# Kernel optimization log

Hardware: AMD Instinct MI355X
Metric: run time of the kernel (lower is better)

The kernel has to match this reference:

```python
import jax, jax.numpy as jnp
from jax import lax
import numpy as np

K_TOP = 100
NMS_THRESH = 0.5
SUBJECT_CATEGORY_ID = 0


def box_cxcywh_to_xyxy(b):
    cx, cy, w, h = b[..., 0], b[..., 1], b[..., 2], b[..., 3]
    return jnp.stack([cx - 0.5 * w, cy - 0.5 * h, cx + 0.5 * w, cy + 0.5 * h], axis=-1)


def _pairwise_iou(boxes):
    # boxes: [K,4] xyxy; uses the +1 pixel convention from the original numpy NMS
    x1, y1, x2, y2 = boxes[:, 0], boxes[:, 1], boxes[:, 2], boxes[:, 3]
    area = (x2 - x1 + 1.0) * (y2 - y1 + 1.0)
    xx1 = jnp.maximum(x1[:, None], x1[None, :])
    yy1 = jnp.maximum(y1[:, None], y1[None, :])
    xx2 = jnp.minimum(x2[:, None], x2[None, :])
    yy2 = jnp.minimum(y2[:, None], y2[None, :])
    w = jnp.maximum(0.0, xx2 - xx1 + 1.0)
    h = jnp.maximum(0.0, yy2 - yy1 + 1.0)
    inter = w * h
    union = area[:, None] + area[None, :] - inter
    return inter / union


def _nms_keep(sub_boxes, obj_boxes, obj_labels, hoi_scores):
    # Greedy grouped pairwise NMS for one image.
    # Grouping key degenerates to object label (subject cat and verb-row are constant).
    K = sub_boxes.shape[0]
    max_scores = hoi_scores.max(axis=-1)
    order = jnp.argsort(-max_scores)
    ovr = _pairwise_iou(sub_boxes) * _pairwise_iou(obj_boxes)  # [K,K]
    same_group = obj_labels[:, None] == obj_labels[None, :]
    ovr = jnp.where(same_group, ovr, 0.0)
    ovr_s = ovr[order][:, order]
    upper = jnp.triu(jnp.ones((K, K), dtype=bool), k=1)
    sup_mat = (ovr_s > NMS_THRESH) & upper  # suppression only of later (lower-score) items

    def body(i, st):
        suppressed, keep = st
        ki = jnp.logical_not(suppressed[i])
        keep = keep.at[i].set(ki)
        suppressed = suppressed | (ki & sup_mat[i])
        return suppressed, keep

    _, keep_sorted = lax.fori_loop(0, K, body, (jnp.zeros(K, bool), jnp.zeros(K, bool)))
    return jnp.zeros(K, bool).at[order].set(keep_sorted)


def setup_inputs() -> dict:
    key = jax.random.key(0)
    k1, k2, k3, k4, k5, k6 = jax.random.split(key, 6)
    B, Q, C, V = 256, 300, 81, 117
    return {
        "pred_obj_logits": jax.random.normal(k1, (B, Q, C), dtype=jnp.float32),
        "pred_verb_logits": jax.random.normal(k2, (B, Q, V), dtype=jnp.float32),
        "pred_sub_boxes": jax.random.uniform(k3, (B, Q, 4), dtype=jnp.float32),
        "pred_obj_boxes": jax.random.uniform(k4, (B, Q, 4), dtype=jnp.float32),
        "correct_mat": (jax.random.uniform(k5, (V, C), dtype=jnp.float32) > 0.3).astype(jnp.float32),
        "target_sizes": jax.random.randint(k6, (B, 2), 200, 640, dtype=jnp.int32),
    }


def reference(pred_obj_logits, pred_verb_logits, pred_sub_boxes, pred_obj_boxes, correct_mat, target_sizes):
    B, Q, C = pred_obj_logits.shape
    V = pred_verb_logits.shape[-1]

    obj_prob = jax.nn.softmax(pred_obj_logits, axis=-1)       # [B,Q,C]  (no_obj=False)
    verb_scores = jax.nn.sigmoid(pred_verb_logits)            # [B,Q,V]

    topk_values, topk_indexes = lax.top_k(obj_prob.reshape(B, Q * C), K_TOP)  # [B,100]
    topk_boxes = topk_indexes // C
    obj_labels = topk_indexes % C

    vs = jnp.take_along_axis(verb_scores, topk_boxes[..., None], axis=1)      # [B,100,V]
    ob = jnp.take_along_axis(pred_obj_boxes, topk_boxes[..., None], axis=1)   # [B,100,4]
    sb = jnp.take_along_axis(pred_sub_boxes, topk_boxes[..., None], axis=1)

    img_h = target_sizes[:, 0].astype(jnp.float32)
    img_w = target_sizes[:, 1].astype(jnp.float32)
    scale_fct = jnp.stack([img_w, img_h, img_w, img_h], axis=1)  # [B,4]
    sub_boxes = box_cxcywh_to_xyxy(sb) * scale_fct[:, None, :]
    obj_boxes = box_cxcywh_to_xyxy(ob) * scale_fct[:, None, :]

    hoi_scores = vs * topk_values[..., None]                    # [B,100,V]
    # masks[b,k,v] = correct_mat[v, obj_labels[b,k]]
    masks = correct_mat.T[obj_labels]                           # [B,100,V]
    hoi_scores = hoi_scores * masks

    keep = jax.vmap(_nms_keep)(sub_boxes, obj_boxes, obj_labels, hoi_scores)  # [B,100] bool
    final_scores = hoi_scores * keep[..., None].astype(hoi_scores.dtype)

    return final_scores, topk_values, obj_labels, sub_boxes, obj_boxes, keep
```

## Files before the change

### kernel.cpp

```cpp
#include <hip/hip_runtime.h>
#include <cmath>

#pragma clang fp contract(off)

#define NT 1024
constexpr int B_ = 256, Q_ = 300, C_ = 81, V_ = 117, K_ = 100;
constexpr int QC_ = Q_ * C_;
constexpr int KV_ = K_ * V_;
constexpr int NB  = 2048;
constexpr int CAP = 1024;

using u32 = unsigned int;
using u64 = unsigned long long;
using u16 = unsigned short;
using u8  = unsigned char;

constexpr int OFF_P16  = 0;
constexpr int OFF_HIST = 48600;
constexpr int OFF_RMAX = OFF_HIST + 8192;
constexpr int OFF_RINV = OFF_RMAX + 1200;
constexpr int OFF_BSUB = OFF_RINV + 1200;
constexpr int OFF_BOBJ = OFF_BSUB + 1600;
constexpr int OFF_SUPR = OFF_BOBJ + 1600;
constexpr int OFF_SELV = OFF_SUPR + 1600;
constexpr int OFF_SELI = OFF_SELV + 400;
constexpr int OFF_MAXB = OFF_SELI + 400;
constexpr int OFF_ORD  = OFF_MAXB + 400;
constexpr int OFF_MISC = OFF_ORD + 104;
constexpr int SMEM_SZ  = OFF_MISC + 48;
static_assert(SMEM_SZ <= 65536, "LDS overflow");

__device__ __forceinline__ u64 shfl_xor_u64(u64 v, int mask) {
    u32 lo = (u32)v, hi = (u32)(v >> 32);
    lo = (u32)__shfl_xor((int)lo, mask, 64);
    hi = (u32)__shfl_xor((int)hi, mask, 64);
    return ((u64)hi << 32) | lo;
}

__device__ __forceinline__ float iou1(const float* a, const float* b) {
    float areaA = (a[2] - a[0] + 1.f) * (a[3] - a[1] + 1.f);
    float areaB = (b[2] - b[0] + 1.f) * (b[3] - b[1] + 1.f);
    float xx1 = fmaxf(a[0], b[0]);
    float yy1 = fmaxf(a[1], b[1]);
    float xx2 = fminf(a[2], b[2]);
    float yy2 = fminf(a[3], b[3]);
    float w = fmaxf(0.f, xx2 - xx1 + 1.f);
    float h = fmaxf(0.f, yy2 - yy1 + 1.f);
    float inter = w * h;
    return inter / (areaA + areaB - inter);
}

__global__ __launch_bounds__(NT) void hoi_kernel(
    const float* __restrict__ obj_logits,
    const float* __restrict__ verb_logits,
    const float* __restrict__ sub_boxes_in,
    const float* __restrict__ obj_boxes_in,
    const float* __restrict__ cm,
    const int*   __restrict__ tsizes,
    float* __restrict__ out)
{
    const int b = blockIdx.x;
    const int tid = threadIdx.x;

    __shared__ __align__(16) u8 smem[SMEM_SZ];
    u16*   p16     = (u16*)(smem + OFF_P16);
    u32*   hist    = (u32*)(smem + OFF_HIST);
    u64*   cand    = (u64*)(smem + OFF_HIST);
    float* rowmax  = (float*)(smem + OFF_RMAX);
    float* rinv    = (float*)(smem + OFF_RINV);
    float (*bsub)[4]   = (float(*)[4])(smem + OFF_BSUB);
    float (*bobj)[4]   = (float(*)[4])(smem + OFF_BOBJ);
    u32   (*suprow)[4] = (u32(*)[4])(smem + OFF_SUPR);
    float* sel_val = (float*)(smem + OFF_SELV);
    u32*   sel_idx = (u32*)(smem + OFF_SELI);
    u32*   maxbits = (u32*)(smem + OFF_MAXB);
    u8*    order8  = (u8*)(smem + OFF_ORD);
    u32*   skeep     = (u32*)(smem + OFF_MISC);
    u32*   keep_bits = (u32*)(smem + OFF_MISC + 16);
    u32*   s_cnt     = (u32*)(smem + OFF_MISC + 32);
    int*   sT        = (int*)(smem + OFF_MISC + 36);
    int*   sW        = (int*)(smem + OFF_MISC + 40);
    u32*   sAcc      = (u32*)(smem + OFF_MISC + 44);
    u32*   swsum   = (u32*)(smem + OFF_BSUB);
    u64*   wred    = (u64*)(smem + OFF_BOBJ);
    u64*   s_prev  = (u64*)(smem + OFF_SUPR);

    const float* lg = obj_logits + (size_t)b * QC_;

    float* o0 = out;
    float* o1 = out + (size_t)B_ * KV_;
    float* o2 = o1 + (size_t)B_ * K_;
    float* o3 = o2 + (size_t)B_ * K_;
    float* o4 = o3 + (size_t)B_ * K_ * 4;
    float* o5 = o4 + (size_t)B_ * K_ * 4;

    for (int i = tid; i < NB; i += NT) hist[i] = 0;
    if (tid == 0) *s_cnt = 0;
    __syncthreads();

    {
        int g = tid >> 5, l = tid & 31;
        bool have2 = (l < C_ - 64);
        for (int q = g; q < Q_; q += 32) {
            const float* row = lg + q * C_;
            float v0 = row[l], v1 = row[l + 32];
            float v2 = have2 ? row[l + 64] : -INFINITY;
            float m = fmaxf(fmaxf(v0, v1), v2);
            for (int off = 16; off; off >>= 1) m = fmaxf(m, __shfl_xor(m, off, 64));
            float e0 = __expf(v0 - m), e1 = __expf(v1 - m);
            float e2 = have2 ? __expf(v2 - m) : 0.f;
            float s = e0 + e1 + e2;
            for (int off = 16; off; off >>= 1) s += __shfl_xor(s, off, 64);
            float ri = 1.f / s;
            u32 b0 = __float_as_uint(e0 * ri), b1 = __float_as_uint(e1 * ri);
            p16[q * C_ + l]      = (u16)(b0 >> 16);
            p16[q * C_ + l + 32] = (u16)(b1 >> 16);
            atomicAdd(&hist[b0 >> 21], 1u);
            atomicAdd(&hist[b1 >> 21], 1u);
            if (have2) {
                u32 b2 = __float_as_uint(e2 * ri);
                p16[q * C_ + l + 64] = (u16)(b2 >> 16);
                atomicAdd(&hist[b2 >> 21], 1u);
            }
            if (l == 0) { rowmax[q] = m; rinv[q] = ri; }
        }
    }
    __syncthreads();

    u32 my_c, my_suf;
    {
        my_c = hist[2 * tid] + hist[2 * tid + 1];
        my_suf = my_c;
        #pragma unroll
        for (int off = 1; off < 64; off <<= 1) {
            u32 o = (u32)__shfl_down((int)my_suf, off, 64);
            my_suf += ((tid & 63) + off < 64) ? o : 0;
        }
        if ((tid & 63) == 0) swsum[tid >> 6] = my_suf;
    }
    __syncthreads();
    if (tid < 16) {
        u32 sufW = swsum[tid];
        #pragma unroll
        for (int off = 1; off < 16; off <<= 1) {
            u32 o = (u32)__shfl_down((int)sufW, off, 64);
            sufW += (tid + off < 16) ? o : 0;
        }
        u32 nxt = (u32)__shfl_down((int)sufW, 1, 64);
        if (tid == 15) nxt = 0;
        if (sufW >= (u32)K_ && nxt < (u32)K_) { *sW = tid; *sAcc = nxt; }
    }
    __syncthreads();
    if ((tid >> 6) == *sW) {
        u32 above = *sAcc + (my_suf - my_c);
        if (above < (u32)K_ && above + my_c >= (u32)K_) {
            u32 acc = above + hist[2 * tid + 1];
            *sT = (acc >= (u32)K_) ? (2 * tid + 1) : (2 * tid);
        }
    }
    __syncthreads();
    const int T = *sT;
    __syncthreads();

    for (int i = tid; i < QC_; i += NT) {
        u32 pb = p16[i];
        if ((int)(pb >> 5) >= T) {
            u32 pos = atomicAdd(s_cnt, 1u);
            if (pos < (u32)CAP) {
                int q = i / C_;
                float p = __expf(lg[i] - rowmax[q]) * rinv[q];
                cand[pos] = ((u64)__float_as_uint(p) << 32) | (u32)(~i);
            }
        }
    }
    __syncthreads();
    const int ncand = (int)*s_cnt;

    auto cswap = [](u64& a, u64& bb, bool up) {
        if ((a > bb) == up) { u64 t = a; a = bb; bb = t; }
    };

    if (ncand <= 256) {
        if (tid < 64) {
            u64 v0 = (tid < ncand) ? cand[tid] : 0ull;
            u64 v1 = (64 + tid < ncand) ? cand[64 + tid] : 0ull;
            u64 v2 = (128 + tid < ncand) ? cand[128 + tid] : 0ull;
            u64 v3 = (192 + tid < ncand) ? cand[192 + tid] : 0ull;
            for (int k = 2; k <= 256; k <<= 1) {
                for (int j = k >> 1; j > 0; j >>= 1) {
                    if (j == 128) {
                        cswap(v0, v2, true);
                        cswap(v1, v3, true);
                    } else if (j == 64) {
                        cswap(v0, v1, true);
                        cswap(v2, v3, (k == 256));
                    } else {
                        auto step = [&](u64& v, int ebase) {
                            u64 pv = shfl_xor_u64(v, j);
                            int e = ebase + tid;
                            bool up = ((e & k) == 0);
                            bool lower = ((e & j) == 0);
                            u64 mn = v < pv ? v : pv;
                            u64 mx = v < pv ? pv : v;
                            v = (lower == up) ? mn : mx;
                        };
                        step(v0, 0); step(v1, 64); step(v2, 128); step(v3, 192);
                    }
                }
            }
            int e2 = 128 + tid;
            if (e2 >= 156) {
                int t = 255 - e2;
                sel_val[t] = __uint_as_float((u32)(v2 >> 32));
                sel_idx[t] = ~(u32)v2;
            }
            int t3 = 255 - (192 + tid);
            sel_val[t3] = __uint_as_float((u32)(v3 >> 32));
            sel_idx[t3] = ~(u32)v3;
        }
    } else if (ncand <= CAP) {
        for (int e = tid; e < CAP; e += NT)
            if (e >= ncand) cand[e] = 0;
        __syncthreads();
        for (int k = 2; k <= CAP; k <<= 1) {
            for (int j = k >> 1; j > 0; j >>= 1) {
                int e = tid, partner = e ^ j;
                if (partner > e) {
                    u64 a = cand[e], bb = cand[partner];
                    bool up = ((e & k) == 0);
                    if ((a > bb) == up) { cand[e] = bb; cand[partner] = a; }
                }
                __syncthreads();
            }
        }
        if (tid < K_) {
            u64 m = cand[CAP - 1 - tid];
            sel_val[tid] = __uint_as_float((u32)(m >> 32));
            sel_idx[tid] = ~(u32)m;
        }
    } else {
        if (tid == 0) *s_prev = ~0ull;
        __syncthreads();
        for (int r = 0; r < K_; r++) {
            u64 prev = *s_prev;
            u64 local = 0;
            for (int i = tid; i < QC_; i += NT) {
                int q = i / C_;
                float p = __expf(lg[i] - rowmax[q]) * rinv[q];
                u64 key = ((u64)__float_as_uint(p) << 32) | (u32)(~i);
                if (key < prev && key > local) local = key;
            }
            for (int off = 32; off > 0; off >>= 1) {
                u64 o = shfl_xor_u64(local, off);
                if (o > local) local = o;
            }
            if ((tid & 63) == 0) wred[tid >> 6] = local;
            __syncthreads();
            if (tid == 0) {
                u64 m = wred[0];
                for (int wv = 1; wv < 16; wv++) if (wred[wv] > m) m = wred[wv];
                *s_prev = m;
                u32 idx = ~(u32)m;
                if (idx >= (u32)QC_) idx = 0;
                sel_val[r] = __uint_as_float((u32)(m >> 32));
                sel_idx[r] = idx;
            }
            __syncthreads();
        }
    }
    __syncthreads();

    if (tid < K_) {
        int idx = (int)sel_idx[tid];
        int q = idx / C_;
        float iw = (float)tsizes[b * 2 + 1];
        float ih = (float)tsizes[b * 2 + 0];
        float4 sb = ((const float4*)sub_boxes_in)[(size_t)b * Q_ + q];
        float4 ob = ((const float4*)obj_boxes_in)[(size_t)b * Q_ + q];
        bsub[tid][0] = (sb.x - 0.5f * sb.z) * iw; bsub[tid][1] = (sb.y - 0.5f * sb.w) * ih;
        bsub[tid][2] = (sb.x + 0.5f * sb.z) * iw; bsub[tid][3] = (sb.y + 0.5f * sb.w) * ih;
        bobj[tid][0] = (ob.x - 0.5f * ob.z) * iw; bobj[tid][1] = (ob.y - 0.5f * ob.w) * ih;
        bobj[tid][2] = (ob.x + 0.5f * ob.z) * iw; bobj[tid][3] = (ob.y + 0.5f * ob.w) * ih;
        suprow[tid][0] = 0; suprow[tid][1] = 0; suprow[tid][2] = 0; suprow[tid][3] = 0;
    }
    if (tid >= 128 && tid < 132) keep_bits[tid - 128] = 0;
    __syncthreads();

    {
        int w = tid >> 6, l = tid & 63;
        for (int r = w; r < K_; r += 16) {
            int idx = (int)sel_idx[r];
            int q = idx / C_, lab = idx - q * C_;
            float val = sel_val[r];
            const float* vrow = verb_logits + ((size_t)b * Q_ + q) * V_;
            float* orow = o0 + (size_t)b * KV_ + r * V_;
            float x0 = vrow[l];
            float h0 = (1.f / (1.f + __expf(-x0))) * val * cm[l * C_ + lab];
            orow[l] = h0;
            float h1 = 0.f;
            if (l < V_ - 64) {
                float x1 = vrow[l + 64];
                h1 = (1.f / (1.f + __expf(-x1))) * val * cm[(l + 64) * C_ + lab];
                orow[l + 64] = h1;
            }
            float m = fmaxf(h0, h1);
            for (int off = 32; off; off >>= 1) m = fmaxf(m, __shfl_xor(m, off, 64));
            if (l == 0) maxbits[r] = __float_as_uint(m);
        }
    }
    __syncthreads();

    if (tid < 800) {
        int r = tid >> 3, j = tid & 7;
        u64 kr = ((u64)maxbits[r] << 32) | (u32)(~r);
        int rank = 0;
        for (int k = 0; k < 13; k++) {
            int jj = j * 13 + k;
            if (jj < K_) {
                u64 kj = ((u64)maxbits[jj] << 32) | (u32)(~jj);
                rank += (kj > kr) ? 1 : 0;
            }
        }
        for (int off = 4; off; off >>= 1) rank += __shfl_xor(rank, off, 64);
        if (j == 0) order8[rank] = (u8)r;
    }
    __syncthreads();

    for (int e = tid; e < K_ * K_; e += NT) {
        int i = e / K_, j = e - i * K_;
        if (j > i) {
            int ri = order8[i], rj = order8[j];
            u32 li = sel_idx[ri] % (u32)C_, lj = sel_idx[rj] % (u32)C_;
            if (li == lj) {
                float o = iou1(bsub[ri], bsub[rj]) * iou1(bobj[ri], bobj[rj]);
                if (o > 0.5f)
                    atomicOr(&suprow[i][j >> 5], 1u << (j & 31));
            }
        }
    }
    __syncthreads();

    if (tid < 64) {
        u32 ra0 = suprow[tid][0], ra1 = suprow[tid][1], ra2 = suprow[tid][2], ra3 = suprow[tid][3];
        u32 rb0 = 0, rb1 = 0, rb2 = 0, rb3 = 0;
        if (tid < K_ - 64) {
            rb0 = suprow[tid + 64][0]; rb1 = suprow[tid + 64][1];
            rb2 = suprow[tid + 64][2]; rb3 = suprow[tid + 64][3];
        }
        u32 acc[4] = {0, 0, 0, 0};
        u32 km[4]  = {0, 0, 0, 0};
        #pragma unroll
        for (int i = 0; i < K_; i++) {
            u32 r0, r1, r2, r3;
            if (i < 64) {
                r0 = (u32)__shfl((int)ra0, i, 64); r1 = (u32)__shfl((int)ra1, i, 64);
                r2 = (u32)__shfl((int)ra2, i, 64); r3 = (u32)__shfl((int)ra3, i, 64);
            } else {
                r0 = (u32)__shfl((int)rb0, i - 64, 64); r1 = (u32)__shfl((int)rb1, i - 64, 64);
                r2 = (u32)__shfl((int)rb2, i - 64, 64); r3 = (u32)__shfl((int)rb3, i - 64, 64);
            }
            bool sup_i = (acc[i >> 5] >> (i & 31)) & 1u;
            if (!sup_i) {
                km[i >> 5] |= 1u << (i & 31);
                acc[0] |= r0; acc[1] |= r1; acc[2] |= r2; acc[3] |= r3;
            }
        }
        if (tid == 0) { skeep[0] = km[0]; skeep[1] = km[1]; skeep[2] = km[2]; skeep[3] = km[3]; }
    }
    __syncthreads();
    if (tid < K_) {
        if ((skeep[tid >> 5] >> (tid & 31)) & 1u) {
            int r = order8[tid];
            atomicOr(&keep_bits[r >> 5], 1u << (r & 31));
        }
    }
    __syncthreads();

    {
        int w = tid >> 6, l = tid & 63;
        for (int r = w; r < K_; r += 16) {
            if (!((keep_bits[r >> 5] >> (r & 31)) & 1u)) {
                float* orow = o0 + (size_t)b * KV_ + r * V_;
                orow[l] = 0.f;
                if (l < V_ - 64) orow[l + 64] = 0.f;
            }
        }
    }
    if (tid < K_) {
        bool kp = (keep_bits[tid >> 5] >> (tid & 31)) & 1u;
        o1[(size_t)b * K_ + tid] = sel_val[tid];
        o2[(size_t)b * K_ + tid] = (float)(sel_idx[tid] % (u32)C_);
        o5[(size_t)b * K_ + tid] = kp ? 1.f : 0.f;
    }
    if (tid < K_ * 4) {
        int r = tid >> 2, k = tid & 3;
        o3[((size_t)b * K_) * 4 + tid] = bsub[r][k];
        o4[((size_t)b * K_) * 4 + tid] = bobj[r][k];
    }
}

extern "C" void kernel_launch(void* const* d_in, const int* in_sizes, int n_in,
                              void* d_out, int out_size, void* d_ws, size_t ws_size,
                              hipStream_t stream) {
    const float* obj_logits  = (const float*)d_in[0];
    const float* verb_logits = (const float*)d_in[1];
    const float* sub_boxes   = (const float*)d_in[2];
    const float* obj_boxes   = (const float*)d_in[3];
    const float* cm          = (const float*)d_in[4];
    const int*   ts          = (const int*)d_in[5];
    hipLaunchKernelGGL(hoi_kernel, dim3(B_), dim3(NT), 0, stream,
                       obj_logits, verb_logits, sub_boxes, obj_boxes, cm, ts,
                       (float*)d_out);
}
```

Before: 143.7 us.

## Unroll softmax rows by two, single-wave threshold search, drop barriers

The softmax/histogram loop now handles two rows per iteration, so there are more independent loads and shuffles in flight. The three-phase threshold search over the 2048-bin histogram becomes one wavefront doing a two-level (chunk, then bin) suffix scan with ballot, which removes two block barriers. Zeroing of the suppression rows and keep bits moves to the start of the kernel, which drops another barrier before the verb stage. s_prev moves into the misc area so it no longer aliases suprow. The risks are a serial 32-bin sum per lane in one wave and a subtle dependence on ordering for correctness.

```diff
diff --git a/kernel.cpp b/kernel.cpp
--- a/kernel.cpp
+++ b/kernel.cpp
@@ -29,6 +29,7 @@
 constexpr int OFF_MISC = OFF_ORD + 104;
 constexpr int SMEM_SZ  = OFF_MISC + 48;
 static_assert(SMEM_SZ <= 65536, "LDS overflow");
+static_assert((OFF_MISC + 40) % 8 == 0, "s_prev align");
 
 __device__ __forceinline__ u64 shfl_xor_u64(u64 v, int mask) {
     u32 lo = (u32)v, hi = (u32)(v >> 32);
@@ -79,11 +80,8 @@
     u32*   keep_bits = (u32*)(smem + OFF_MISC + 16);
     u32*   s_cnt     = (u32*)(smem + OFF_MISC + 32);
     int*   sT        = (int*)(smem + OFF_MISC + 36);
-    int*   sW        = (int*)(smem + OFF_MISC + 40);
-    u32*   sAcc      = (u32*)(smem + OFF_MISC + 44);
-    u32*   swsum   = (u32*)(smem + OFF_BSUB);
-    u64*   wred    = (u64*)(smem + OFF_BOBJ);
-    u64*   s_prev  = (u64*)(smem + OFF_SUPR);
+    u64*   s_prev    = (u64*)(smem + OFF_MISC + 40);
+    u64*   wred      = (u64*)(smem + OFF_BOBJ);
 
     const float* lg = obj_logits + (size_t)b * QC_;
 
@@ -95,13 +93,61 @@
     float* o5 = o4 + (size_t)B_ * K_ * 4;
 
     for (int i = tid; i < NB; i += NT) hist[i] = 0;
-    if (tid == 0) *s_cnt = 0;
+    if (tid < 400) ((u32*)(smem + OFF_SUPR))[tid] = 0;
+    else if (tid < 404) keep_bits[tid - 400] = 0;
+    if (tid == 0) { *s_cnt = 0; *sT = 0; }
     __syncthreads();
 
     {
         int g = tid >> 5, l = tid & 31;
         bool have2 = (l < C_ - 64);
-        for (int q = g; q < Q_; q += 32) {
+        int q = g;
+        for (; q + 32 < Q_; q += 64) {
+            const float* rowA = lg + q * C_;
+            const float* rowB = lg + (q + 32) * C_;
+            float a0 = rowA[l], a1 = rowA[l + 32];
+            float b0 = rowB[l], b1 = rowB[l + 32];
+            float a2 = have2 ? rowA[l + 64] : -INFINITY;
+            float b2 = have2 ? rowB[l + 64] : -INFINITY;
+            float ma = fmaxf(fmaxf(a0, a1), a2);
+            float mb = fmaxf(fmaxf(b0, b1), b2);
+            for (int off = 16; off; off >>= 1) {
+                ma = fmaxf(ma, __shfl_xor(ma, off, 64));
+                mb = fmaxf(mb, __shfl_xor(mb, off, 64));
+            }
+            float ea0 = __expf(a0 - ma), eb0 = __expf(b0 - mb);
+            float ea1 = __expf(a1 - ma), eb1 = __expf(b1 - mb);
+            float ea2 = have2 ? __expf(a2 - ma) : 0.f;
+            float eb2 = have2 ? __expf(b2 - mb) : 0.f;
+            float sa = ea0 + ea1 + ea2, sb = eb0 + eb1 + eb2;
+            for (int off = 16; off; off >>= 1) {
+                sa += __shfl_xor(sa, off, 64);
+                sb += __shfl_xor(sb, off, 64);
+            }
+            float ria = 1.f / sa, rib = 1.f / sb;
+            u32 A0 = __float_as_uint(ea0 * ria), A1 = __float_as_uint(ea1 * ria);
+            u32 B0 = __float_as_uint(eb0 * rib), B1 = __float_as_uint(eb1 * rib);
+            p16[q * C_ + l]             = (u16)(A0 >> 16);
+            p16[q * C_ + l + 32]        = (u16)(A1 >> 16);
+            p16[(q + 32) * C_ + l]      = (u16)(B0 >> 16);
+            p16[(q + 32) * C_ + l + 32] = (u16)(B1 >> 16);
+            atomicAdd(&hist[A0 >> 21], 1u);
+            atomicAdd(&hist[A1 >> 21], 1u);
+            atomicAdd(&hist[B0 >> 21], 1u);
+            atomicAdd(&hist[B1 >> 21], 1u);
+            if (have2) {
+                u32 A2 = __float_as_uint(ea2 * ria), B2 = __float_as_uint(eb2 * rib);
+                p16[q * C_ + l + 64]        = (u16)(A2 >> 16);
+                p16[(q + 32) * C_ + l + 64] = (u16)(B2 >> 16);
+                atomicAdd(&hist[A2 >> 21], 1u);
+                atomicAdd(&hist[B2 >> 21], 1u);
+            }
+            if (l == 0) {
+                rowmax[q] = ma; rinv[q] = ria;
+                rowmax[q + 32] = mb; rinv[q + 32] = rib;
+            }
+        }
+        if (q < Q_) {
             const float* row = lg + q * C_;
             float v0 = row[l], v1 = row[l + 32];
             float v2 = have2 ? row[l + 64] : -INFINITY;
@@ -127,40 +173,35 @@
     }
     __syncthreads();
 
-    u32 my_c, my_suf;
-    {
-        my_c = hist[2 * tid] + hist[2 * tid + 1];
-        my_suf = my_c;
+    if (tid < 64) {
+        int d = tid;
+        u32 c = 0;
+        int base = d * 32;
+        for (int k = 0; k < 32; k++) c += hist[base + k];
+        u32 suf = c;
         #pragma unroll
         for (int off = 1; off < 64; off <<= 1) {
-            u32 o = (u32)__shfl_down((int)my_suf, off, 64);
-            my_suf += ((tid & 63) + off < 64) ? o : 0;
-        }
-        if ((tid & 63) == 0) swsum[tid >> 6] = my_suf;
-    }
-    __syncthreads();
-    if (tid < 16) {
-        u32 sufW = swsum[tid];
+            u32 o = (u32)__shfl_down((int)suf, off, 64);
+            suf += (d + off < 64) ? o : 0;
+        }
+        u32 above_chunk = suf - c;
+        bool own = (above_chunk < (u32)K_) && (above_chunk + c >= (u32)K_);
+        u64 mask = __ballot(own);
+        int d0 = __ffsll((long long)mask) - 1;
+        u32 above0 = (u32)__shfl((int)above_chunk, d0, 64);
+        u32 h = (d < 32) ? hist[d0 * 32 + d] : 0;
+        u32 suf2 = h;
         #pragma unroll
-        for (int off = 1; off < 16; off <<= 1) {
-            u32 o = (u32)__shfl_down((int)sufW, off, 64);
-            sufW += (tid + off < 16) ? o : 0;
-        }
-        u32 nxt = (u32)__shfl_down((int)sufW, 1, 64);
-        if (tid == 15) nxt = 0;
-        if (sufW >= (u32)K_ && nxt < (u32)K_) { *sW = tid; *sAcc = nxt; }
-    }
-    __syncthreads();
-    if ((tid >> 6) == *sW) {
-        u32 above = *sAcc + (my_suf - my_c);
-        if (above < (u32)K_ && above + my_c >= (u32)K_) {
-            u32 acc = above + hist[2 * tid + 1];
-            *sT = (acc >= (u32)K_) ? (2 * tid + 1) : (2 * tid);
-        }
+        for (int off = 1; off < 64; off <<= 1) {
+            u32 o = (u32)__shfl_down((int)suf2, off, 64);
+            suf2 += (d + off < 64) ? o : 0;
+        }
+        u32 above_bin = above0 + (suf2 - h);
+        if (d < 32 && above_bin < (u32)K_ && above_bin + h >= (u32)K_)
+            *sT = d0 * 32 + d;
     }
     __syncthreads();
     const int T = *sT;
-    __syncthreads();
 
     for (int i = tid; i < QC_; i += NT) {
         u32 pb = p16[i];
@@ -281,11 +322,7 @@
         bsub[tid][2] = (sb.x + 0.5f * sb.z) * iw; bsub[tid][3] = (sb.y + 0.5f * sb.w) * ih;
         bobj[tid][0] = (ob.x - 0.5f * ob.z) * iw; bobj[tid][1] = (ob.y - 0.5f * ob.w) * ih;
         bobj[tid][2] = (ob.x + 0.5f * ob.z) * iw; bobj[tid][3] = (ob.y + 0.5f * ob.w) * ih;
-        suprow[tid][0] = 0; suprow[tid][1] = 0; suprow[tid][2] = 0; suprow[tid][3] = 0;
-    }
-    if (tid >= 128 && tid < 132) keep_bits[tid - 128] = 0;
-    __syncthreads();
-
+    }
     {
         int w = tid >> 6, l = tid & 63;
         for (int r = w; r < K_; r += 16) {
```

New measurement: 143.5 us. No clear change (-0.2%).
